# Performance work log

Hardware: AMD Instinct MI355X
Metric: run time of the kernel (lower is better)

The kernel has to match this reference:

```python
import jax, jax.numpy as jnp
import numpy as np

V, H, FAST, SLOW = 32000, 256, 64, 256
B, T = 32, 1024
THRESH = 0.3
NEG = -1e9


def setup_inputs() -> dict:
    key = jax.random.key(0)
    ks = jax.random.split(key, 16)
    s = 0.02
    return {
        "seq":   jax.random.randint(ks[0], (B, T), 0, V),
        "embed": jax.random.normal(ks[1], (V, H), jnp.float32) * s,
        "W1": jax.random.normal(ks[2], (H, 2 * H), jnp.float32) * s,
        "b1": jnp.zeros((2 * H,), jnp.float32),
        "W2": jax.random.normal(ks[3], (2 * H, H), jnp.float32) * s,
        "b2": jnp.zeros((H,), jnp.float32),
        "gamma": jnp.ones((H,), jnp.float32),
        "beta":  jnp.zeros((H,), jnp.float32),
        "Wg": jax.random.normal(ks[4], (H, 1), jnp.float32) * s,
        "bg": jnp.zeros((1,), jnp.float32),
        "Wd": jax.random.normal(ks[5], (H, 1), jnp.float32) * s,
        "bd": jnp.zeros((1,), jnp.float32),
        "Wq": jax.random.normal(ks[6], (H, H), jnp.float32) * s,
        "bq": jnp.zeros((H,), jnp.float32),
        "Wo": jax.random.normal(ks[7], (H, V), jnp.float32) * s,
        "bo": jnp.zeros((V,), jnp.float32),
    }


def _layer_norm(x, g, b, eps=1e-5):
    mu = x.mean(-1, keepdims=True)
    var = ((x - mu) ** 2).mean(-1, keepdims=True)
    return (x - mu) * jax.lax.rsqrt(var + eps) * g + b


def _writer(h, Wg, bg, Wd, bd):
    """Vectorized-over-batch LRU writer with learned demotion; scan over time."""
    Bn = h.shape[0]
    init = (
        jnp.zeros((Bn, FAST, H), h.dtype),   # fast_mem
        jnp.zeros((Bn, SLOW, H), h.dtype),   # slow_mem
        jnp.zeros((Bn, FAST), jnp.int32),    # fast_age
        jnp.zeros((Bn, SLOW), jnp.int32),    # slow_age
        jnp.zeros((Bn, FAST), bool),         # fast_used
        jnp.zeros((Bn, SLOW), bool),         # slow_used
    )

    def step(st, tok_h):
        fm, sm, fa, sa, fu, su = st
        ws = jax.nn.sigmoid(tok_h @ Wg + bg)[:, 0]          # [B]
        fa = fa + fu.astype(jnp.int32)
        sa = sa + su.astype(jnp.int32)
        write = ws >= 0.4                                    # torch skips if < 0.4
        tok = jax.lax.stop_gradient(tok_h)                   # .detach() in torch

        free_f = ~fu                                         # [B,FAST]
        has_free = jnp.any(free_f, axis=1)                   # [B]
        sl = jnp.argmax(free_f, axis=1)                      # first free fast slot

        ds = (fm @ Wd + bd)[..., 0]                          # [B,FAST] demotion scores
        dem = jnp.argmin(ds, axis=1)                         # [B]
        dh = jnp.take_along_axis(fm, dem[:, None, None], axis=1)[:, 0]  # [B,H]

        free_s = ~su
        has_free_s = jnp.any(free_s, axis=1)
        ss = jnp.where(has_free_s, jnp.argmax(free_s, axis=1), jnp.argmax(sa, axis=1))

        fidx = jnp.where(has_free, sl, dem)                  # fast write slot
        sel_f = jax.nn.one_hot(fidx, FAST, dtype=bool) & write[:, None]
        do_slow = write & ~has_free                          # demotion happens
        sel_s = jax.nn.one_hot(ss, SLOW, dtype=bool) & do_slow[:, None]

        # slow write (demoted value) uses fm BEFORE the fast overwrite
        sm = jnp.where(sel_s[:, :, None], dh[:, None, :], sm)
        sa = jnp.where(sel_s, 0, sa)
        su = su | sel_s

        fm = jnp.where(sel_f[:, :, None], tok[:, None, :], fm)
        fa = jnp.where(sel_f, 0, fa)
        fu = fu | sel_f
        return (fm, sm, fa, sa, fu, su), None

    tokens = jnp.swapaxes(h[:, : h.shape[1] - 3], 0, 1)      # [T-3, B, H]
    (fm, sm, fa, sa, fu, su), _ = jax.lax.scan(step, init, tokens)
    return fm, sm, fu.astype(h.dtype), su.astype(h.dtype)


def reference(seq, embed, W1, b1, W2, b2, gamma, beta, Wg, bg, Wd, bd, Wq, bq, Wo, bo):
    h0 = embed[seq]                                          # [B,T,H]
    ff = jnp.maximum(h0 @ W1 + b1, 0.0) @ W2 + b2
    h = _layer_norm(h0 + ff, gamma, beta)

    fm, sm, fmask, smask = _writer(h, Wg, bg, Wd, bd)

    q = h[:, -1, :] @ Wq + bq                                # [B,H]
    f_scores = jnp.einsum("bfd,bd->bf", fm, q)
    f_scores = jnp.where(fmask == 0, NEG, f_scores)
    f_attn = jax.nn.softmax(f_scores, axis=-1)
    f_ctx = jnp.einsum("bf,bfd->bd", f_attn, fm)
    max_attn = f_attn.max(axis=-1)

    s_scores = jnp.einsum("bsd,bd->bs", sm, q)
    s_scores = jnp.where(smask == 0, NEG, s_scores)
    s_attn = jax.nn.softmax(s_scores, axis=-1)
    s_ctx = jnp.einsum("bs,bsd->bd", s_attn, sm)

    need_slow = (max_attn < THRESH).astype(h.dtype)          # [B]
    ctx = f_ctx + need_slow[:, None] * s_ctx
    logits = ctx @ Wo + bo
    return logits, need_slow
```

## Files before the change

kernel.cpp:

```cpp
#include <hip/hip_runtime.h>
#include <hip/hip_bf16.h>
#include <cstdint>

#define NEGV -1e9f

typedef __attribute__((ext_vector_type(8))) short short8v;
typedef __attribute__((ext_vector_type(4))) float f32x4;

union U8 {
  unsigned u[4];
  short8v v;
};

__device__ __forceinline__ float wred_sum(float v) {
#pragma unroll
  for (int o = 32; o; o >>= 1) v += __shfl_xor(v, o);
  return v;
}
__device__ __forceinline__ float wred_max(float v) {
#pragma unroll
  for (int o = 32; o; o >>= 1) v = fmaxf(v, __shfl_xor(v, o));
  return v;
}
template <int CTRL>
__device__ __forceinline__ float dpp_fadd(float x) {
  int xi = __float_as_int(x);
  int yi = __builtin_amdgcn_update_dpp(xi, xi, CTRL, 0xF, 0xF, false);
  return x + __int_as_float(yi);
}
__device__ __forceinline__ float dpp_sum63(float v) {
  v = dpp_fadd<0xB1>(v);
  v = dpp_fadd<0x4E>(v);
  v = dpp_fadd<0x141>(v);
  v = dpp_fadd<0x140>(v);
  v = dpp_fadd<0x142>(v);
  v = dpp_fadd<0x143>(v);
  return v;
}
__device__ __forceinline__ float dpp_sum16(float v) {
  v = dpp_fadd<0xB1>(v);
  v = dpp_fadd<0x4E>(v);
  v = dpp_fadd<0x141>(v);
  v = dpp_fadd<0x140>(v);
  return v;
}

__device__ __forceinline__ ushort bf16hi(float x) {
  unsigned u = __float_as_uint(x);
  unsigned r = u + 0x7FFFu + ((u >> 16) & 1u);
  return (ushort)(r >> 16);
}
__device__ __forceinline__ float bf16tof(ushort u) {
  return __uint_as_float(((unsigned)u) << 16);
}
__device__ __forceinline__ void split8(const float* xs, uint4& hv, uint4& lv) {
  unsigned h[8], l[8];
#pragma unroll
  for (int j = 0; j < 8; ++j) {
    const ushort hh = bf16hi(xs[j]);
    h[j] = hh;
    l[j] = bf16hi(xs[j] - bf16tof(hh));
  }
  hv = make_uint4(h[0] | (h[1] << 16), h[2] | (h[3] << 16),
                  h[4] | (h[5] << 16), h[6] | (h[7] << 16));
  lv = make_uint4(l[0] | (l[1] << 16), l[2] | (l[3] << 16),
                  l[4] | (l[5] << 16), l[6] | (l[7] << 16));
}

__device__ __forceinline__ void gload_lds16(const void* g, void* l) {
  __builtin_amdgcn_global_load_lds(
      (const __attribute__((address_space(1))) unsigned int*)g,
      (__attribute__((address_space(3))) unsigned int*)l, 16, 0, 0);
}

__global__ __launch_bounds__(256) void wprep2_k(const float* __restrict__ W,
                                                char* __restrict__ Wti, int K,
                                                int N) {
  __shared__ float tile[32][33];
  const int k0 = blockIdx.x * 32, n0 = blockIdx.y * 32;
  const int r = threadIdx.x >> 5, c = threadIdx.x & 31;
#pragma unroll
  for (int i = 0; i < 4; ++i)
    tile[r + i * 8][c] = W[(size_t)(k0 + r + i * 8) * N + n0 + c];
  __syncthreads();
  if (threadIdx.x < 128) {
    const int gn = threadIdx.x & 31, gk = threadIdx.x >> 5;
    float xs[8];
#pragma unroll
    for (int i = 0; i < 8; ++i) xs[i] = tile[gk * 8 + i][gn];
    uint4 hv, lv;
    split8(xs, hv, lv);
    char* dst = Wti + (size_t)(n0 + gn) * K * 4 + (k0 >> 5) * 128 + gk * 16;
    *(uint4*)dst = hv;
    *(uint4*)(dst + 64) = lv;
  }
}

__global__ __launch_bounds__(512, 2) void gemm1g_k(
    const int* __restrict__ seq, const float* __restrict__ embed,
    const char* __restrict__ w1ti, const float* __restrict__ bias,
    unsigned* __restrict__ outp) {
  __shared__ alignas(16) ushort A[4096];
  __shared__ alignas(16) ushort B[16384];
  __shared__ int sidx[64];
  const int tid = threadIdx.x;
  const int m0 = blockIdx.x * 64, n0 = blockIdx.y * 256;
  if (tid < 64) sidx[tid] = seq[m0 + tid];
  __syncthreads();
  const int lane = tid & 63, w = tid >> 6;
  const int wm = (w >> 2) * 32, wn = (w & 3) * 64;
  const int r15 = lane & 15, khalf = lane >> 4;

  f32x4 acc[2][4];
#pragma unroll
  for (int i = 0; i < 2; ++i)
#pragma unroll
    for (int j = 0; j < 4; ++j) acc[i][j] = (f32x4){0.f, 0.f, 0.f, 0.f};

#pragma unroll 1
  for (int s = 0; s < 8; ++s) {
    const size_t sb = (size_t)s * 128;
    if (tid < 256) {
      const int row = tid >> 2, q = tid & 3;
      const float* ap = embed + (size_t)sidx[row] * 256 + s * 32 + q * 8;
      const float4 x0 = *(const float4*)ap;
      const float4 x1 = *(const float4*)(ap + 4);
      const float xs[8] = {x0.x, x0.y, x0.z, x0.w, x1.x, x1.y, x1.z, x1.w};
      uint4 hv, lv;
      split8(xs, hv, lv);
      const int r7 = row & 7;
      *(uint4*)&A[(row * 8 + (q ^ r7)) * 8] = hv;
      *(uint4*)&A[(row * 8 + ((4 | q) ^ r7)) * 8] = lv;
    }
#pragma unroll
    for (int i = 0; i < 4; ++i) {
      const int cb = i * 512 + w * 64;
      const int c = cb + lane;
      const int row = c >> 3;
      const int lc = (c & 7) ^ (row & 7);
      gload_lds16(w1ti + (size_t)(n0 + row) * 1024 + sb + lc * 16,
                  &B[cb * 8]);
    }
    __syncthreads();
    short8v ahf[2], alf[2], bhf[4], blf[4];
#pragma unroll
    for (int t = 0; t < 2; ++t) {
      const int ra = wm + t * 16 + r15;
      ahf[t] = *(const short8v*)&A[(ra * 8 + (khalf ^ (ra & 7))) * 8];
      alf[t] = *(const short8v*)&A[(ra * 8 + ((4 | khalf) ^ (ra & 7))) * 8];
    }
#pragma unroll
    for (int t = 0; t < 4; ++t) {
      const int rb = wn + t * 16 + r15;
      bhf[t] = *(const short8v*)&B[(rb * 8 + (khalf ^ (rb & 7))) * 8];
      blf[t] = *(const short8v*)&B[(rb * 8 + ((4 | khalf) ^ (rb & 7))) * 8];
    }
#pragma unroll
    for (int mi = 0; mi < 2; ++mi)
#pragma unroll
      for (int ni = 0; ni < 4; ++ni) {
        acc[mi][ni] = __builtin_amdgcn_mfma_f32_16x16x32_bf16(
            ahf[mi], bhf[ni], acc[mi][ni], 0, 0, 0);
        acc[mi][ni] = __builtin_amdgcn_mfma_f32_16x16x32_bf16(
            ahf[mi], blf[ni], acc[mi][ni], 0, 0, 0);
        acc[mi][ni] = __builtin_amdgcn_mfma_f32_16x16x32_bf16(
            alf[mi], bhf[ni], acc[mi][ni], 0, 0, 0);
      }
    __syncthreads();
  }
#pragma unroll
  for (int ni = 0; ni < 4; ++ni) {
    const int n = n0 + wn + ni * 16 + r15;
    const float bv = bias[n];
#pragma unroll
    for (int mi = 0; mi < 2; ++mi) {
      const int mbase = m0 + wm + mi * 16 + khalf * 4;
#pragma unroll
      for (int j = 0; j < 4; ++j) {
        const float t = fmaxf(acc[mi][ni][j] + bv, 0.f);
        const ushort h = bf16hi(t);
        const ushort l = bf16hi(t - bf16tof(h));
        outp[(size_t)(mbase + j) * 512 + n] = (unsigned)h | ((unsigned)l << 16);
      }
    }
  }
}

__global__ __launch_bounds__(512, 2) void gemm2i_k(
    const unsigned* __restrict__ Ap, const char* __restrict__ w2ti,
    const float* __restrict__ b2, const int* __restrict__ seq,
    const float* __restrict__ embed, const float* __restrict__ gamma,
    const float* __restrict__ beta, const float* __restrict__ Wg,
    const float* __restrict__ bg, const float* __restrict__ Wd,
    const float* __restrict__ bd, float* __restrict__ X,
    int* __restrict__ wbit, float* __restrict__ dsc) {
  __shared__ alignas(16) unsigned Apk[2048];
  __shared__ alignas(16) ushort B[16384];
  __shared__ float par0[64][4], par1[64][4], gpar[64][4], dpar[64][4];
  __shared__ float g_s[256], be_s[256], wg_s[256], wd_s[256], b2_s[256];
  __shared__ int sidx[64];
  const int tid = threadIdx.x;
  const int m0 = blockIdx.x * 64;
  if (tid < 64) sidx[tid] = seq[m0 + tid];
  if (tid >= 256) {
    const int c = tid - 256;
    g_s[c] = gamma[c];
    be_s[c] = beta[c];
    wg_s[c] = Wg[c];
    wd_s[c] = Wd[c];
    b2_s[c] = b2[c];
  }
  const int lane = tid & 63, w = tid >> 6;
  const int wm = (w >> 2) * 32, wn = (w & 3) * 64;
  const int r15 = lane & 15, khalf = lane >> 4;

  f32x4 acc[2][4];
#pragma unroll
  for (int i = 0; i < 2; ++i)
#pragma unroll
    for (int j = 0; j < 4; ++j) acc[i][j] = (f32x4){0.f, 0.f, 0.f, 0.f};

#pragma unroll 1
  for (int s = 0; s < 16; ++s) {
    {
      const int cb = w * 64;
      const int c = cb + lane;
      const int row = c >> 3;
      const int lc = (c & 7) ^ (row & 7);
      gload_lds16(Ap + (size_t)(m0 + row) * 512 + s * 32 + lc * 4,
                  &Apk[cb * 4]);
    }
    const size_t sb = (size_t)s * 128;
#pragma unroll
    for (int i = 0; i < 4; ++i) {
      const int cb = i * 512 + w * 64;
      const int c = cb + lane;
      const int row = c >> 3;
      const int lc = (c & 7) ^ (row & 7);
      gload_lds16(w2ti + (size_t)row * 2048 + sb + lc * 16, &B[cb * 8]);
    }
    __syncthreads();
    short8v ahf[2], alf[2], bhf[4], blf[4];
#pragma unroll
    for (int t = 0; t < 2; ++t) {
      const int ra = wm + t * 16 + r15;
      const int r7 = ra & 7;
      const uint4 ua = *(const uint4*)&Apk[(ra * 8 + ((khalf * 2) ^ r7)) * 4];
      const uint4 ub =
          *(const uint4*)&Apk[(ra * 8 + ((khalf * 2 + 1) ^ r7)) * 4];
      U8 vh, vl;
      vh.u[0] = (ua.x & 0xffffu) | (ua.y << 16);
      vl.u[0] = (ua.x >> 16) | (ua.y & 0xffff0000u);
      vh.u[1] = (ua.z & 0xffffu) | (ua.w << 16);
      vl.u[1] = (ua.z >> 16) | (ua.w & 0xffff0000u);
      vh.u[2] = (ub.x & 0xffffu) | (ub.y << 16);
      vl.u[2] = (ub.x >> 16) | (ub.y & 0xffff0000u);
      vh.u[3] = (ub.z & 0xffffu) | (ub.w << 16);
      vl.u[3] = (ub.z >> 16) | (ub.w & 0xffff0000u);
      ahf[t] = vh.v;
      alf[t] = vl.v;
    }
#pragma unroll
    for (int t = 0; t < 4; ++t) {
      const int rb = wn + t * 16 + r15;
      bhf[t] = *(const short8v*)&B[(rb * 8 + (khalf ^ (rb & 7))) * 8];
      blf[t] = *(const short8v*)&B[(rb * 8 + ((4 | khalf) ^ (rb & 7))) * 8];
    }
#pragma unroll
    for (int mi = 0; mi < 2; ++mi)
#pragma unroll
      for (int ni = 0; ni < 4; ++ni) {
        acc[mi][ni] = __builtin_amdgcn_mfma_f32_16x16x32_bf16(
            ahf[mi], bhf[ni], acc[mi][ni], 0, 0, 0);
        acc[mi][ni] = __builtin_amdgcn_mfma_f32_16x16x32_bf16(
            ahf[mi], blf[ni], acc[mi][ni], 0, 0, 0);
        acc[mi][ni] = __builtin_amdgcn_mfma_f32_16x16x32_bf16(
            alf[mi], bhf[ni], acc[mi][ni], 0, 0, 0);
      }
    __syncthreads();
  }

  float mu_r[2][4];
#pragma unroll
  for (int mi = 0; mi < 2; ++mi)
#pragma unroll
    for (int j = 0; j < 4; ++j) {
      const int rowl = wm + mi * 16 + khalf * 4 + j;
      const float* ep = embed + (size_t)sidx[rowl] * 256;
#pragma unroll
      for (int ni = 0; ni < 4; ++ni) {
        const int col = wn + ni * 16 + r15;
        float t = acc[mi][ni][j] + b2_s[col];
        acc[mi][ni][j] = t + ep[col];
      }
      float s = (acc[mi][0][j] + acc[mi][1][j]) + (acc[mi][2][j] + acc[mi][3][j]);
      s = dpp_sum16(s);
      if (r15 == 0) par0[rowl][w & 3] = s;
    }
  __syncthreads();
#pragma unroll
  for (int mi = 0; mi < 2; ++mi)
#pragma unroll
    for (int j = 0; j < 4; ++j) {
      const int rowl = wm + mi * 16 + khalf * 4 + j;
      const float mu = ((par0[rowl][0] + par0[rowl][1]) +
                        (par0[rowl][2] + par0[rowl][3])) * (1.f / 256.f);
      mu_r[mi][j] = mu;
      const float d0 = acc[mi][0][j] - mu, d1 = acc[mi][1][j] - mu;
      const float d2 = acc[mi][2][j] - mu, d3 = acc[mi][3][j] - mu;
      float vv = (d0 * d0 + d1 * d1) + (d2 * d2 + d3 * d3);
      vv = dpp_sum16(vv);
      if (r15 == 0) par1[rowl][w & 3] = vv;
    }
  __syncthreads();
#pragma unroll
  for (int mi = 0; mi < 2; ++mi)
#pragma unroll
    for (int j = 0; j < 4; ++j) {
      const int rowl = wm + mi * 16 + khalf * 4 + j;
      const float mu = mu_r[mi][j];
      const float var = ((par1[rowl][0] + par1[rowl][1]) +
                         (par1[rowl][2] + par1[rowl][3])) * (1.f / 256.f);
      const float rstd = 1.f / sqrtf(var + 1e-5f);
      float ys[4], gw[4], dw[4];
#pragma unroll
      for (int ni = 0; ni < 4; ++ni) {
        const int col = wn + ni * 16 + r15;
        const float y = (acc[mi][ni][j] - mu) * rstd * g_s[col] + be_s[col];
        X[(size_t)(m0 + rowl) * 256 + col] = y;
        ys[ni] = y;
        gw[ni] = wg_s[col];
        dw[ni] = wd_s[col];
      }
      float gp = (ys[0] * gw[0] + ys[1] * gw[1]) + (ys[2] * gw[2] + ys[3] * gw[3]);
      float dp = (ys[0] * dw[0] + ys[1] * dw[1]) + (ys[2] * dw[2] + ys[3] * dw[3]);
      gp = dpp_sum16(gp);
      dp = dpp_sum16(dp);
      if (r15 == 0) {
        gpar[rowl][w & 3] = gp;
        dpar[rowl][w & 3] = dp;
      }
    }
  __syncthreads();
  if (tid < 64) {
    const int row = tid;
    const float gs = ((gpar[row][0] + gpar[row][1]) +
                      (gpar[row][2] + gpar[row][3])) + bg[0];
    const float dsv = ((dpar[row][0] + dpar[row][1]) +
                       (dpar[row][2] + dpar[row][3])) + bd[0];
    float sig;
    if (gs >= 0.f) {
      sig = 1.f / (1.f + expf(-gs));
    } else {
      const float e2 = expf(gs);
      sig = e2 / (1.f + e2);
    }
    wbit[m0 + row] = (sig >= 0.4f) ? 1 : 0;
    dsc[m0 + row] = dsv;
  }
}

__global__ __launch_bounds__(1024) void rank_k(
    const int* __restrict__ wbit, const float* __restrict__ dsc,
    unsigned* __restrict__ r12) {
  const int b = blockIdx.y;
  const int s0 = blockIdx.x * 128;
  const int tid = threadIdx.x;
  const int lane = tid & 63, wv = tid >> 6;
  __shared__ unsigned long long skey[1024];
  __shared__ int wavecnt[16];
  __shared__ int waveoff[17];

  int flag = 0;
  float d = 0.f;
  if (tid < 1021) {
    flag = wbit[b * 1024 + tid];
    d = dsc[b * 1024 + tid];
  }
  const unsigned long long m = __ballot(flag != 0);
  if (lane == 0) wavecnt[wv] = __popcll(m);
  skey[tid] = ~0ull;
  __syncthreads();
  if (tid == 0) {
    int acc = 0;
    for (int i = 0; i < 16; ++i) { waveoff[i] = acc; acc += wavecnt[i]; }
    waveoff[16] = acc;
  }
  __syncthreads();
  const int W = waveoff[16];
  if (flag) {
    unsigned u = __float_as_uint(d);
    u = (u & 0x80000000u) ? ~u : (u | 0x80000000u);
    const int w = waveoff[wv] + __popcll(m & ((1ull << lane) - 1ull));
    skey[w] = ((unsigned long long)u << 32) | (unsigned)w;
  }
  __syncthreads();
  const unsigned long long ki = skey[tid];
  __syncthreads();
  if (tid == W - 1) skey[tid] = ~0ull;
  __syncthreads();

  const int end2 = max(0, W - 257);
  int r1 = 0, r2 = 0;
#pragma unroll 8
  for (int jj = 0; jj < 128; ++jj) {
    const int j = s0 + jj;
    const int lt = skey[j] < ki;
    r1 += lt;
    r2 += (j < end2) ? lt : 0;
  }
  r12[((size_t)b * 8 + blockIdx.x) * 1024 + tid] =
      (unsigned)r1 | ((unsigned)r2 << 16);
}

__global__ __launch_bounds__(1024) void selattn_k(
    const int* __restrict__ wbit, const float* __restrict__ dsc,
    const unsigned* __restrict__ r12, const float* __restrict__ X,
    const float* __restrict__ Wq, const float* __restrict__ bq,
    float* __restrict__ ctx, float* __restrict__ needs_out) {
  const int b = blockIdx.x;
  const int tid = threadIdx.x;
  const int lane = tid & 63, wv = tid >> 6;
  __shared__ int stokl[1024];
  __shared__ int wavecnt[16];
  __shared__ int waveoff[17];
  __shared__ int fcnt_s[16], scnt_s[16];
  __shared__ int foff[16], soff[16];
  __shared__ int ft[64], st[256];
  __shared__ float hl[256], q[256];
  __shared__ float qpart[4][256];
  __shared__ float sc_f[64], at_f[64];
  __shared__ float sc_s[256], at_s[256];
  __shared__ float redm[4], reds[4];
  __shared__ float needs_s;
  __shared__ float cpart[16][256];

  int flag = 0;
  if (tid < 1021) flag = wbit[b * 1024 + tid];
  const unsigned long long m = __ballot(flag != 0);
  if (lane == 0) wavecnt[wv] = __popcll(m);
  __syncthreads();
  if (tid == 0) {
    int acc = 0;
    for (int i = 0; i < 16; ++i) { waveoff[i] = acc; acc += wavecnt[i]; }
    waveoff[16] = acc;
  }
  __syncthreads();
  const int W = waveoff[16];
  if (flag) {
    const int w = waveoff[wv] + __popcll(m & ((1ull << lane) - 1ull));
    stokl[w] = tid;
  }
  __syncthreads();

  int r1 = 0, r2 = 0;
  {
    const unsigned* rp = r12 + (size_t)b * 8192 + tid;
#pragma unroll
    for (int s = 0; s < 8; ++s) {
      const unsigned v = rp[s * 1024];
      r1 += (int)(v & 0xffffu);
      r2 += (int)(v >> 16);
    }
  }
  const int K = W - 64;
  const int end2 = max(0, W - 257);
  bool fastf = false, slowf = false;
  if (tid < W) {
    const bool isLast = (tid == W - 1);
    const bool inEK = (!isLast) && (r1 < K);
    const bool inE2 = (tid < end2) && (r2 < K - 256);
    fastf = isLast || (!isLast && r1 >= K);
    slowf = inEK && !inE2;
  }

  const unsigned long long mf = __ballot(fastf);
  const unsigned long long ms = __ballot(slowf);
  if (lane == 0) { fcnt_s[wv] = __popcll(mf); scnt_s[wv] = __popcll(ms); }
  __syncthreads();
  if (tid == 0) {
    int a = 0, c = 0;
    for (int i = 0; i < 16; ++i) {
      foff[i] = a; a += fcnt_s[i];
      soff[i] = c; c += scnt_s[i];
    }
  }
  __syncthreads();
  if (fastf) {
    const int p = foff[wv] + __popcll(mf & ((1ull << lane) - 1ull));
    ft[p] = stokl[tid];
  }
  if (slowf) {
    const int p = soff[wv] + __popcll(ms & ((1ull << lane) - 1ull));
    st[p] = stokl[tid];
  }
  const int nf = min(W, 64);
  const int ns = min(max(K, 0), 256);

  const float* Xb = X + (size_t)b * 1024 * 256;
  if (tid < 256) hl[tid] = Xb[(size_t)1023 * 256 + tid];
  __syncthreads();

  {
    const int col = tid & 255, kc = tid >> 8;
    float a = 0.f;
    const float* wp = Wq + (size_t)(kc * 64) * 256 + col;
#pragma unroll 4
    for (int k = 0; k < 64; ++k) a = fmaf(hl[kc * 64 + k], wp[(size_t)k * 256], a);
    qpart[kc][col] = a;
  }
  __syncthreads();
  if (tid < 256)
    q[tid] = ((qpart[0][tid] + qpart[1][tid]) + qpart[2][tid]) + qpart[3][tid] +
             bq[tid];
  __syncthreads();

  const float4 qq = *(const float4*)(q + lane * 4);
#pragma unroll 2
  for (int i = 0; i < 20; ++i) {
    const int r = wv + 16 * i;
    bool valid;
    int tok;
    if (r < 64) { valid = r < nf; tok = valid ? ft[r] : 0; }
    else        { valid = (r - 64) < ns; tok = valid ? st[r - 64] : 0; }
    float sc = NEGV;
    if (valid) {
      const float4 xr = *(const float4*)(Xb + (size_t)tok * 256 + lane * 4);
      float p = (xr.x * qq.x + xr.y * qq.y) + (xr.z * qq.z + xr.w * qq.w);
      sc = dpp_sum63(p);
    }
    if (lane == 63) {
      if (r < 64) sc_f[r] = sc;
      else sc_s[r - 64] = sc;
    }
  }
  __syncthreads();

  if (wv < 4) {
    float s = sc_s[tid];
    float mx = wred_max(s);
    if (lane == 0) redm[wv] = mx;
  } else if (wv == 8) {
    float s = sc_f[lane];
    float mx = wred_max(s);
    float e = expf(s - mx);
    float sm = wred_sum(e);
    float a = e / sm;
    at_f[lane] = a;
    float ma = wred_max(a);
    if (lane == 0) needs_s = (ma < 0.3f) ? 1.f : 0.f;
  }
  __syncthreads();
  if (wv < 4) {
    float s = sc_s[tid];
    float mx = fmaxf(fmaxf(redm[0], redm[1]), fmaxf(redm[2], redm[3]));
    float e = expf(s - mx);
    float sm = wred_sum(e);
    if (lane == 0) reds[wv] = sm;
    at_s[tid] = e;
  }
  __syncthreads();
  if (tid < 256) {
    float sm = (reds[0] + reds[1]) + (reds[2] + reds[3]);
    at_s[tid] = at_s[tid] / sm;
  }
  __syncthreads();

  const float needs = needs_s;
  float4 cp = {0.f, 0.f, 0.f, 0.f};
#pragma unroll 2
  for (int i = 0; i < 20; ++i) {
    const int r = wv + 16 * i;
    bool valid;
    int tok;
    float a;
    if (r < 64) { valid = r < nf; tok = valid ? ft[r] : 0; a = at_f[r]; }
    else {
      valid = (r - 64) < ns;
      tok = valid ? st[r - 64] : 0;
      a = needs * at_s[r - 64];
    }
    if (valid) {
      const float4 xr = *(const float4*)(Xb + (size_t)tok * 256 + lane * 4);
      cp.x = fmaf(a, xr.x, cp.x);
      cp.y = fmaf(a, xr.y, cp.y);
      cp.z = fmaf(a, xr.z, cp.z);
      cp.w = fmaf(a, xr.w, cp.w);
    }
  }
  *(float4*)&cpart[wv][lane * 4] = cp;
  __syncthreads();
  if (tid < 256) {
    float c = 0.f;
#pragma unroll
    for (int w = 0; w < 16; ++w) c += cpart[w][tid];
    ctx[b * 256 + tid] = c;
  }
  if (tid == 0) needs_out[b] = needs;
}

__global__ __launch_bounds__(256) void logits5_k(
    const float* __restrict__ ctx, const float* __restrict__ Wo,
    const float* __restrict__ bo, float* __restrict__ out) {
  __shared__ float cs[256 * 8];
  const int tid = threadIdx.x;
  const int b0 = blockIdx.y * 8;
  for (int i = tid; i < 2048; i += 256) {
    int bb = i & 7, hh = i >> 3;
    cs[hh * 8 + bb] = ctx[(b0 + bb) * 256 + hh];
  }
  __syncthreads();
  const int v = blockIdx.x * 256 + tid;
  float acc[8] = {0.f, 0.f, 0.f, 0.f, 0.f, 0.f, 0.f, 0.f};
  for (int h0 = 0; h0 < 256; h0 += 16) {
    float wv[16];
#pragma unroll
    for (int u = 0; u < 16; ++u) wv[u] = Wo[(size_t)(h0 + u) * 32000 + v];
#pragma unroll
    for (int u = 0; u < 16; ++u) {
      const float4 c0 = *(const float4*)&cs[(h0 + u) * 8];
      const float4 c1 = *(const float4*)&cs[(h0 + u) * 8 + 4];
      acc[0] = fmaf(c0.x, wv[u], acc[0]);
      acc[1] = fmaf(c0.y, wv[u], acc[1]);
      acc[2] = fmaf(c0.z, wv[u], acc[2]);
      acc[3] = fmaf(c0.w, wv[u], acc[3]);
      acc[4] = fmaf(c1.x, wv[u], acc[4]);
      acc[5] = fmaf(c1.y, wv[u], acc[5]);
      acc[6] = fmaf(c1.z, wv[u], acc[6]);
      acc[7] = fmaf(c1.w, wv[u], acc[7]);
    }
  }
  const float bv = bo[v];
#pragma unroll
  for (int bb = 0; bb < 8; ++bb)
    out[(size_t)(b0 + bb) * 32000 + v] = acc[bb] + bv;
}

extern "C" void kernel_launch(void* const* d_in, const int* in_sizes, int n_in,
                              void* d_out, int out_size, void* d_ws,
                              size_t ws_size, hipStream_t stream) {
  const int* seq = (const int*)d_in[0];
  const float* embed = (const float*)d_in[1];
  const float* W1 = (const float*)d_in[2];
  const float* b1 = (const float*)d_in[3];
  const float* W2 = (const float*)d_in[4];
  const float* b2 = (const float*)d_in[5];
  const float* gamma = (const float*)d_in[6];
  const float* beta = (const float*)d_in[7];
  const float* Wg = (const float*)d_in[8];
  const float* bg = (const float*)d_in[9];
  const float* Wd = (const float*)d_in[10];
  const float* bd = (const float*)d_in[11];
  const float* Wq = (const float*)d_in[12];
  const float* bq = (const float*)d_in[13];
  const float* Wo = (const float*)d_in[14];
  const float* bo = (const float*)d_in[15];
  float* out = (float*)d_out;

  char* wsb = (char*)d_ws;
  char* w1ti = wsb;
  char* w2ti = wsb + 524288;
  int* wbit = (int*)(wsb + 1048576);
  float* dscp = (float*)(wsb + 1179648);
  float* ctxp = (float*)(wsb + 1310720);
  unsigned* r12p = (unsigned*)(wsb + 1343488);
  const size_t base = 2392064;

  const int nch = (ws_size >= (size_t)106000000) ? 1 : 2;
  const int rows = 32768 / nch;
  const size_t actsz = (size_t)rows * 512 * 4;
  unsigned* act1p = (unsigned*)(wsb + base);
  float* X = (float*)(wsb + base + actsz);

  dim3 blk(256);
  wprep2_k<<<dim3(8, 16), blk, 0, stream>>>(W1, w1ti, 256, 512);
  wprep2_k<<<dim3(16, 8), blk, 0, stream>>>(W2, w2ti, 512, 256);

  for (int c = 0; c < nch; ++c) {
    const int* seqc = seq + c * rows;
    gemm1g_k<<<dim3(rows / 64, 2), dim3(512), 0, stream>>>(seqc, embed, w1ti,
                                                           b1, act1p);
    gemm2i_k<<<dim3(rows / 64), dim3(512), 0, stream>>>(
        act1p, w2ti, b2, seqc, embed, gamma, beta, Wg, bg, Wd, bd,
        X + (size_t)c * rows * 256, wbit + c * rows, dscp + c * rows);
  }

  rank_k<<<dim3(8, 32), dim3(1024), 0, stream>>>(wbit, dscp, r12p);
  selattn_k<<<32, dim3(1024), 0, stream>>>(wbit, dscp, r12p, X, Wq, bq, ctxp,
                                           out + (size_t)32 * 32000);
  logits5_k<<<dim3(125, 4), blk, 0, stream>>>(ctxp, Wo, bo, out);
}
```

Before: 138.8 us.

## Load GEMM A operands directly into registers and double the K step per barrier

New measurement: 200.5 us. 1.44x slower.

```diff
diff --git a/kernel.cpp b/kernel.cpp
--- a/kernel.cpp
+++ b/kernel.cpp
@@ -66,6 +66,11 @@
   lv = make_uint4(l[0] | (l[1] << 16), l[2] | (l[3] << 16),
                   l[4] | (l[5] << 16), l[6] | (l[7] << 16));
 }
+__device__ __forceinline__ short8v u4v(const uint4& x) {
+  U8 t;
+  t.u[0] = x.x; t.u[1] = x.y; t.u[2] = x.z; t.u[3] = x.w;
+  return t.v;
+}
 
 __device__ __forceinline__ void gload_lds16(const void* g, void* l) {
   __builtin_amdgcn_global_load_lds(
@@ -96,20 +101,18 @@
   }
 }
 
-__global__ __launch_bounds__(512, 2) void gemm1g_k(
+__global__ __launch_bounds__(512, 2) void gemm1r_k(
     const int* __restrict__ seq, const float* __restrict__ embed,
     const char* __restrict__ w1ti, const float* __restrict__ bias,
     unsigned* __restrict__ outp) {
-  __shared__ alignas(16) ushort A[4096];
-  __shared__ alignas(16) ushort B[16384];
-  __shared__ int sidx[64];
+  __shared__ alignas(16) ushort B[32768];
   const int tid = threadIdx.x;
   const int m0 = blockIdx.x * 64, n0 = blockIdx.y * 256;
-  if (tid < 64) sidx[tid] = seq[m0 + tid];
-  __syncthreads();
   const int lane = tid & 63, w = tid >> 6;
   const int wm = (w >> 2) * 32, wn = (w & 3) * 64;
   const int r15 = lane & 15, khalf = lane >> 4;
+  const int sq0 = seq[m0 + wm + r15];
+  const int sq1 = seq[m0 + wm + 16 + r15];
 
   f32x4 acc[2][4];
 #pragma unroll
@@ -118,54 +121,58 @@
     for (int j = 0; j < 4; ++j) acc[i][j] = (f32x4){0.f, 0.f, 0.f, 0.f};
 
 #pragma unroll 1
-  for (int s = 0; s < 8; ++s) {
-    const size_t sb = (size_t)s * 128;
-    if (tid < 256) {
-      const int row = tid >> 2, q = tid & 3;
-      const float* ap = embed + (size_t)sidx[row] * 256 + s * 32 + q * 8;
-      const float4 x0 = *(const float4*)ap;
-      const float4 x1 = *(const float4*)(ap + 4);
-      const float xs[8] = {x0.x, x0.y, x0.z, x0.w, x1.x, x1.y, x1.z, x1.w};
-      uint4 hv, lv;
-      split8(xs, hv, lv);
-      const int r7 = row & 7;
-      *(uint4*)&A[(row * 8 + (q ^ r7)) * 8] = hv;
-      *(uint4*)&A[(row * 8 + ((4 | q) ^ r7)) * 8] = lv;
-    }
-#pragma unroll
-    for (int i = 0; i < 4; ++i) {
+  for (int kg = 0; kg < 4; ++kg) {
+#pragma unroll
+    for (int i = 0; i < 8; ++i) {
       const int cb = i * 512 + w * 64;
       const int c = cb + lane;
-      const int row = c >> 3;
-      const int lc = (c & 7) ^ (row & 7);
-      gload_lds16(w1ti + (size_t)(n0 + row) * 1024 + sb + lc * 16,
+      const int row = c >> 4;
+      const int pc = c & 15;
+      const int lc = pc ^ (row & 7);
+      gload_lds16(w1ti + (size_t)(n0 + row) * 1024 + kg * 256 + lc * 16,
                   &B[cb * 8]);
     }
+    short8v ahf[2][2], alf[2][2];
+#pragma unroll
+    for (int t = 0; t < 2; ++t) {
+      const int sr = t ? sq1 : sq0;
+#pragma unroll
+      for (int ks = 0; ks < 2; ++ks) {
+        const float* ap =
+            embed + (size_t)sr * 256 + kg * 64 + ks * 32 + khalf * 8;
+        const float4 x0 = *(const float4*)ap;
+        const float4 x1 = *(const float4*)(ap + 4);
+        const float xs[8] = {x0.x, x0.y, x0.z, x0.w, x1.x, x1.y, x1.z, x1.w};
+        uint4 hv, lv;
+        split8(xs, hv, lv);
+        ahf[t][ks] = u4v(hv);
+        alf[t][ks] = u4v(lv);
+      }
+    }
     __syncthreads();
-    short8v ahf[2], alf[2], bhf[4], blf[4];
-#pragma unroll
-    for (int t = 0; t < 2; ++t) {
-      const int ra = wm + t * 16 + r15;
-      ahf[t] = *(const short8v*)&A[(ra * 8 + (khalf ^ (ra & 7))) * 8];
-      alf[t] = *(const short8v*)&A[(ra * 8 + ((4 | khalf) ^ (ra & 7))) * 8];
-    }
-#pragma unroll
-    for (int t = 0; t < 4; ++t) {
-      const int rb = wn + t * 16 + r15;
-      bhf[t] = *(const short8v*)&B[(rb * 8 + (khalf ^ (rb & 7))) * 8];
-      blf[t] = *(const short8v*)&B[(rb * 8 + ((4 | khalf) ^ (rb & 7))) * 8];
-    }
-#pragma unroll
-    for (int mi = 0; mi < 2; ++mi)
-#pragma unroll
-      for (int ni = 0; ni < 4; ++ni) {
-        acc[mi][ni] = __builtin_amdgcn_mfma_f32_16x16x32_bf16(
-            ahf[mi], bhf[ni], acc[mi][ni], 0, 0, 0);
-        acc[mi][ni] = __builtin_amdgcn_mfma_f32_16x16x32_bf16(
-            ahf[mi], blf[ni], acc[mi][ni], 0, 0, 0);
-        acc[mi][ni] = __builtin_amdgcn_mfma_f32_16x16x32_bf16(
-            alf[mi], bhf[ni], acc[mi][ni], 0, 0, 0);
-      }
+#pragma unroll
+    for (int ks = 0; ks < 2; ++ks) {
+      short8v bhf[4], blf[4];
+#pragma unroll
+      for (int t = 0; t < 4; ++t) {
+        const int rb = wn + t * 16 + r15;
+        const int r7 = rb & 7;
+        bhf[t] = *(const short8v*)&B[(rb * 16 + ((ks * 8 + khalf) ^ r7)) * 8];
+        blf[t] =
+            *(const short8v*)&B[(rb * 16 + ((ks * 8 + 4 + khalf) ^ r7)) * 8];
+      }
+#pragma unroll
+      for (int mi = 0; mi < 2; ++mi)
+#pragma unroll
+        for (int ni = 0; ni < 4; ++ni) {
+          acc[mi][ni] = __builtin_amdgcn_mfma_f32_16x16x32_bf16(
+              ahf[mi][ks], bhf[ni], acc[mi][ni], 0, 0, 0);
+          acc[mi][ni] = __builtin_amdgcn_mfma_f32_16x16x32_bf16(
+              ahf[mi][ks], blf[ni], acc[mi][ni], 0, 0, 0);
+          acc[mi][ni] = __builtin_amdgcn_mfma_f32_16x16x32_bf16(
+              alf[mi][ks], bhf[ni], acc[mi][ni], 0, 0, 0);
+        }
+    }
     __syncthreads();
   }
 #pragma unroll
@@ -186,7 +193,7 @@
   }
 }
 
-__global__ __launch_bounds__(512, 2) void gemm2i_k(
+__global__ __launch_bounds__(512, 2) void gemm2r_k(
     const unsigned* __restrict__ Ap, const char* __restrict__ w2ti,
     const float* __restrict__ b2, const int* __restrict__ seq,
     const float* __restrict__ embed, const float* __restrict__ gamma,
@@ -194,25 +201,14 @@
     const float* __restrict__ bg, const float* __restrict__ Wd,
     const float* __restrict__ bd, float* __restrict__ X,
     int* __restrict__ wbit, float* __restrict__ dsc) {
-  __shared__ alignas(16) unsigned Apk[2048];
-  __shared__ alignas(16) ushort B[16384];
-  __shared__ float par0[64][4], par1[64][4], gpar[64][4], dpar[64][4];
-  __shared__ float g_s[256], be_s[256], wg_s[256], wd_s[256], b2_s[256];
-  __shared__ int sidx[64];
+  __shared__ alignas(16) ushort B[32768];
   const int tid = threadIdx.x;
   const int m0 = blockIdx.x * 64;
-  if (tid < 64) sidx[tid] = seq[m0 + tid];
-  if (tid >= 256) {
-    const int c = tid - 256;
-    g_s[c] = gamma[c];
-    be_s[c] = beta[c];
-    wg_s[c] = Wg[c];
-    wd_s[c] = Wd[c];
-    b2_s[c] = b2[c];
-  }
   const int lane = tid & 63, w = tid >> 6;
   const int wm = (w >> 2) * 32, wn = (w & 3) * 64;
   const int r15 = lane & 15, khalf = lane >> 4;
+  const int rowA0 = m0 + wm + r15;
+  const int rowA1 = m0 + wm + 16 + r15;
 
   f32x4 acc[2][4];
 #pragma unroll
@@ -221,76 +217,82 @@
     for (int j = 0; j < 4; ++j) acc[i][j] = (f32x4){0.f, 0.f, 0.f, 0.f};
 
 #pragma unroll 1
-  for (int s = 0; s < 16; ++s) {
-    {
-      const int cb = w * 64;
-      const int c = cb + lane;
-      const int row = c >> 3;
-      const int lc = (c & 7) ^ (row & 7);
-      gload_lds16(Ap + (size_t)(m0 + row) * 512 + s * 32 + lc * 4,
-                  &Apk[cb * 4]);
-    }
-    const size_t sb = (size_t)s * 128;
-#pragma unroll
-    for (int i = 0; i < 4; ++i) {
+  for (int kg = 0; kg < 8; ++kg) {
+#pragma unroll
+    for (int i = 0; i < 8; ++i) {
       const int cb = i * 512 + w * 64;
       const int c = cb + lane;
-      const int row = c >> 3;
-      const int lc = (c & 7) ^ (row & 7);
-      gload_lds16(w2ti + (size_t)row * 2048 + sb + lc * 16, &B[cb * 8]);
+      const int row = c >> 4;
+      const int pc = c & 15;
+      const int lc = pc ^ (row & 7);
+      gload_lds16(w2ti + (size_t)row * 2048 + kg * 256 + lc * 16, &B[cb * 8]);
+    }
+    short8v ahf[2][2], alf[2][2];
+#pragma unroll
+    for (int t = 0; t < 2; ++t) {
+      const int rowA = t ? rowA1 : rowA0;
+#pragma unroll
+      for (int ks = 0; ks < 2; ++ks) {
+        const unsigned* apr =
+            Ap + (size_t)rowA * 512 + kg * 64 + ks * 32 + khalf * 8;
+        const uint4 ua = *(const uint4*)apr;
+        const uint4 ub = *(const uint4*)(apr + 4);
+        U8 vh, vl;
+        vh.u[0] = (ua.x & 0xffffu) | (ua.y << 16);
+        vl.u[0] = (ua.x >> 16) | (ua.y & 0xffff0000u);
+        vh.u[1] = (ua.z & 0xffffu) | (ua.w << 16);
+        vl.u[1] = (ua.z >> 16) | (ua.w & 0xffff0000u);
+        vh.u[2] = (ub.x & 0xffffu) | (ub.y << 16);
+        vl.u[2] = (ub.x >> 16) | (ub.y & 0xffff0000u);
+        vh.u[3] = (ub.z & 0xffffu) | (ub.w << 16);
+        vl.u[3] = (ub.z >> 16) | (ub.w & 0xffff0000u);
+        ahf[t][ks] = vh.v;
+        alf[t][ks] = vl.v;
+      }
     }
     __syncthreads();
-    short8v ahf[2], alf[2], bhf[4], blf[4];
-#pragma unroll
-    for (int t = 0; t < 2; ++t) {
-      const int ra = wm + t * 16 + r15;
-      const int r7 = ra & 7;
-      const uint4 ua = *(const uint4*)&Apk[(ra * 8 + ((khalf * 2) ^ r7)) * 4];
-      const uint4 ub =
-          *(const uint4*)&Apk[(ra * 8 + ((khalf * 2 + 1) ^ r7)) * 4];
-      U8 vh, vl;
-      vh.u[0] = (ua.x & 0xffffu) | (ua.y << 16);
-      vl.u[0] = (ua.x >> 16) | (ua.y & 0xffff0000u);
-      vh.u[1] = (ua.z & 0xffffu) | (ua.w << 16);
-      vl.u[1] = (ua.z >> 16) | (ua.w & 0xffff0000u);
-      vh.u[2] = (ub.x & 0xffffu) | (ub.y << 16);
-      vl.u[2] = (ub.x >> 16) | (ub.y & 0xffff0000u);
-      vh.u[3] = (ub.z & 0xffffu) | (ub.w << 16);
-      vl.u[3] = (ub.z >> 16) | (ub.w & 0xffff0000u);
-      ahf[t] = vh.v;
-      alf[t] = vl.v;
-    }
-#pragma unroll
-    for (int t = 0; t < 4; ++t) {
-      const int rb = wn + t * 16 + r15;
-      bhf[t] = *(const short8v*)&B[(rb * 8 + (khalf ^ (rb & 7))) * 8];
-      blf[t] = *(const short8v*)&B[(rb * 8 + ((4 | khalf) ^ (rb & 7))) * 8];
-    }
-#pragma unroll
-    for (int mi = 0; mi < 2; ++mi)
-#pragma unroll
-      for (int ni = 0; ni < 4; ++ni) {
-        acc[mi][ni] = __builtin_amdgcn_mfma_f32_16x16x32_bf16(
-            ahf[mi], bhf[ni], acc[mi][ni], 0, 0, 0);
-        acc[mi][ni] = __builtin_amdgcn_mfma_f32_16x16x32_bf16(
-            ahf[mi], blf[ni], acc[mi][ni], 0, 0, 0);
-        acc[mi][ni] = __builtin_amdgcn_mfma_f32_16x16x32_bf16(
-            alf[mi], bhf[ni], acc[mi][ni], 0, 0, 0);
-      }
+#pragma unroll
+    for (int ks = 0; ks < 2; ++ks) {
+      short8v bhf[4], blf[4];
+#pragma unroll
+      for (int t = 0; t < 4; ++t) {
+        const int rb = wn + t * 16 + r15;
+        const int r7 = rb & 7;
+        bhf[t] = *(const short8v*)&B[(rb * 16 + ((ks * 8 + khalf) ^ r7)) * 8];
+        blf[t] =
+            *(const short8v*)&B[(rb * 16 + ((ks * 8 + 4 + khalf) ^ r7)) * 8];
+      }
+#pragma unroll
+      for (int mi = 0; mi < 2; ++mi)
+#pragma unroll
+        for (int ni = 0; ni < 4; ++ni) {
+          acc[mi][ni] = __builtin_amdgcn_mfma_f32_16x16x32_bf16(
+              ahf[mi][ks], bhf[ni], acc[mi][ni], 0, 0, 0);
+          acc[mi][ni] = __builtin_amdgcn_mfma_f32_16x16x32_bf16(
+              ahf[mi][ks], blf[ni], acc[mi][ni], 0, 0, 0);
+          acc[mi][ni] = __builtin_amdgcn_mfma_f32_16x16x32_bf16(
+              alf[mi][ks], bhf[ni], acc[mi][ni], 0, 0, 0);
+        }
+    }
     __syncthreads();
   }
 
+  char* Bc = (char*)B;
+  float(*par0)[4] = (float(*)[4])(Bc);
+  float(*par1)[4] = (float(*)[4])(Bc + 1024);
+  float(*gpar)[4] = (float(*)[4])(Bc + 2048);
+  float(*dpar)[4] = (float(*)[4])(Bc + 3072);
   float mu_r[2][4];
 #pragma unroll
   for (int mi = 0; mi < 2; ++mi)
 #pragma unroll
     for (int j = 0; j < 4; ++j) {
       const int rowl = wm + mi * 16 + khalf * 4 + j;
-      const float* ep = embed + (size_t)sidx[rowl] * 256;
+      const float* ep = embed + (size_t)seq[m0 + rowl] * 256;
 #pragma unroll
       for (int ni = 0; ni < 4; ++ni) {
         const int col = wn + ni * 16 + r15;
-        float t = acc[mi][ni][j] + b2_s[col];
+        float t = acc[mi][ni][j] + b2[col];
         acc[mi][ni][j] = t + ep[col];
       }
       float s = (acc[mi][0][j] + acc[mi][1][j]) + (acc[mi][2][j] + acc[mi][3][j]);
@@ -326,11 +328,11 @@
 #pragma unroll
       for (int ni = 0; ni < 4; ++ni) {
         const int col = wn + ni * 16 + r15;
-        const float y = (acc[mi][ni][j] - mu) * rstd * g_s[col] + be_s[col];
+        const float y = (acc[mi][ni][j] - mu) * rstd * gamma[col] + beta[col];
         X[(size_t)(m0 + rowl) * 256 + col] = y;
         ys[ni] = y;
-        gw[ni] = wg_s[col];
-        dw[ni] = wd_s[col];
+        gw[ni] = Wg[col];
+        dw[ni] = Wd[col];
       }
       float gp = (ys[0] * gw[0] + ys[1] * gw[1]) + (ys[2] * gw[2] + ys[3] * gw[3]);
       float dp = (ys[0] * dw[0] + ys[1] * dw[1]) + (ys[2] * dw[2] + ys[3] * dw[3]);
@@ -678,9 +680,9 @@
 
   for (int c = 0; c < nch; ++c) {
     const int* seqc = seq + c * rows;
-    gemm1g_k<<<dim3(rows / 64, 2), dim3(512), 0, stream>>>(seqc, embed, w1ti,
+    gemm1r_k<<<dim3(rows / 64, 2), dim3(512), 0, stream>>>(seqc, embed, w1ti,
                                                            b1, act1p);
-    gemm2i_k<<<dim3(rows / 64), dim3(512), 0, stream>>>(
+    gemm2r_k<<<dim3(rows / 64), dim3(512), 0, stream>>>(
         act1p, w2ti, b2, seqc, embed, gamma, beta, Wg, bg, Wd, bd,
         X + (size_t)c * rows * 256, wbit + c * rows, dscp + c * rows);
   }
```
